# Optimization experiments

Measured on AMD Instinct MI355X. Metric: run time of the kernel, lower is better.

The kernel has to match this reference:

```python
import jax, jax.numpy as jnp
import numpy as np

N_ROLES = 6
EPS = 1e-5

def _ln(x, scale, bias):
    m = jnp.mean(x, axis=-1, keepdims=True)
    v = jnp.var(x, axis=-1, keepdims=True)
    return (x - m) * jax.lax.rsqrt(v + EPS) * scale + bias

def setup_inputs() -> dict:
    key = jax.random.key(0)
    ks = jax.random.split(key, 20)
    T, B, D_OBS, H, A = 32, 1024, 256, 512, 32
    inp = {
        'rnn_states': jax.random.normal(ks[0], (B, H), jnp.float32),
        'obs': jax.random.normal(ks[1], (T, B, D_OBS), jnp.float32),
        'resets': jnp.zeros((T, B), jnp.float32),
        'available_actions': jnp.ones((T, B, A), jnp.float32),
        'role_ids': jax.random.randint(ks[2], (T, B), 0, N_ROLES, jnp.int32),
        # feature norm over obs_dim
        'fn_scale': jnp.ones((D_OBS,), jnp.float32),
        'fn_bias': jnp.zeros((D_OBS,), jnp.float32),
        # base MLP: obs_dim->512->512, each followed by LayerNorm
        'W0': jax.random.normal(ks[3], (D_OBS, H), jnp.float32) * 0.02,
        'b0': jnp.zeros((H,), jnp.float32),
        'ln0_scale': jnp.ones((H,), jnp.float32),
        'ln0_bias': jnp.zeros((H,), jnp.float32),
        'W1': jax.random.normal(ks[4], (H, H), jnp.float32) * 0.02,
        'b1': jnp.zeros((H,), jnp.float32),
        'ln1_scale': jnp.ones((H,), jnp.float32),
        'ln1_bias': jnp.zeros((H,), jnp.float32),
        # per-role routes: obs_dim->128->H (stacked over roles)
        'Wr0': jax.random.normal(ks[5], (N_ROLES, D_OBS, 128), jnp.float32) * 0.02,
        'br0': jnp.zeros((N_ROLES, 128), jnp.float32),
        'Wr1': jax.random.normal(ks[6], (N_ROLES, 128, H), jnp.float32) * 0.02,
        'br1': jnp.zeros((N_ROLES, H), jnp.float32),
        # per-role heads: H->64->32->action_dim (stacked over roles)
        'Wh0': jax.random.normal(ks[7], (N_ROLES, H, 64), jnp.float32) * 0.02,
        'bh0': jnp.zeros((N_ROLES, 64), jnp.float32),
        'Wh1': jax.random.normal(ks[8], (N_ROLES, 64, 32), jnp.float32) * 0.02,
        'bh1': jnp.zeros((N_ROLES, 32), jnp.float32),
        'Wh2': jax.random.normal(ks[9], (N_ROLES, 32, A), jnp.float32) * 0.02,
        'bh2': jnp.zeros((N_ROLES, A), jnp.float32),
    }
    return inp

def _gather_by_role(all_values, role_ids):
    # all_values: (K, T, B, F); role_ids: (T, B) -> (T, B, F)
    idx = role_ids[None, :, :, None].astype(jnp.int32)
    return jnp.take_along_axis(all_values, idx, axis=0)[0]

def reference(rnn_states, obs, resets, available_actions, role_ids,
              fn_scale, fn_bias, W0, b0, ln0_scale, ln0_bias,
              W1, b1, ln1_scale, ln1_bias,
              Wr0, br0, Wr1, br1,
              Wh0, bh0, Wh1, bh1, Wh2, bh2):
    # feature normalization on raw obs
    obs_n = _ln(obs, fn_scale, fn_bias)
    # shared base MLP (relu + LayerNorm after each Dense)
    e = _ln(jax.nn.relu(obs_n @ W0 + b0), ln0_scale, ln0_bias)
    e = _ln(jax.nn.relu(e @ W1 + b1), ln1_scale, ln1_bias)
    # per-role pre-GRU residual routes on (normalized) obs
    r = jax.nn.relu(jnp.einsum('tbi,kih->ktbh', obs_n, Wr0) + br0[:, None, None, :])
    r = jax.nn.relu(jnp.einsum('ktbh,kho->ktbo', r, Wr1) + br1[:, None, None, :])
    e = e + _gather_by_role(r, role_ids)
    # no recurrent policy configured: rnn_states pass through
    # per-role heads -> all logits (K, T, B, A)
    h = jax.nn.relu(jnp.einsum('tbh,khf->ktbf', e, Wh0) + bh0[:, None, None, :])
    h = jax.nn.relu(jnp.einsum('ktbf,kfg->ktbg', h, Wh1) + bh1[:, None, None, :])
    all_logits = jnp.einsum('ktbg,kga->ktba', h, Wh2) + bh2[:, None, None, :]
    logits = _gather_by_role(all_logits, role_ids)
    logits = jnp.where(available_actions > 0.5, logits, jnp.full_like(logits, -1e10))
    return rnn_states, logits
```

## Files before the change

### kernel.cpp

```cpp
#include <hip/hip_runtime.h>
#include <stdint.h>

typedef unsigned short u16;
typedef unsigned int u32;

using bf16x8 = __attribute__((ext_vector_type(8))) short;
using f32x4  = __attribute__((ext_vector_type(4))) float;

#define DEVINL __device__ __forceinline__

DEVINL float b2f(u16 u) { return __builtin_bit_cast(float, (u32)u << 16); }
DEVINL u16 f2b(float f) {
  u32 u = __builtin_bit_cast(u32, f);
  u += 0x7FFFu + ((u >> 16) & 1u);
  return (u16)(u >> 16);
}

DEVINL void gll16(const u16* src, u16* dst) {
  __builtin_amdgcn_global_load_lds(
      (const __attribute__((address_space(1))) void*)(uintptr_t)src,
      (__attribute__((address_space(3))) void*)(uintptr_t)dst, 16, 0, 0);
}

DEVINL void tp_tile(const float* __restrict__ s, u16* __restrict__ d,
                    int R, int C, int bx, int by, int z)
{
  __shared__ u16 tile[32][33];
  const size_t mstride = (size_t)R * C;
  s += (size_t)z * mstride;
  d += (size_t)z * mstride;
  int r0 = bx * 32, c0 = by * 32;
  int tx = threadIdx.x & 31, ty = threadIdx.x >> 5;
#pragma unroll
  for (int i = 0; i < 32; i += 8)
    tile[ty + i][tx] = f2b(s[(size_t)(r0 + ty + i) * C + (c0 + tx)]);
  __syncthreads();
#pragma unroll
  for (int i = 0; i < 32; i += 8)
    d[(size_t)(c0 + ty + i) * R + (r0 + tx)] = tile[tx][ty + i];
}

__global__ __launch_bounds__(256) void transpose_all(
    const float* W0, const float* W1, const float* Wr0, const float* Wr1, const float* Wh0,
    u16* W0t, u16* W1t, u16* Wr0t, u16* Wr1t, u16* Wh0t)
{
  int b = blockIdx.x;
  if (b < 128)      {            tp_tile(W0, W0t, 256, 512, b % 8,  b / 8, 0); }
  else if (b < 384) { b -= 128;  tp_tile(W1, W1t, 512, 512, b % 16, b / 16, 0); }
  else if (b < 576) { b -= 384;  int t = b / 8;  tp_tile(Wr0, Wr0t, 256, 128, b % 8,  t % 4,  t / 4); }
  else if (b < 960) { b -= 576;  int t = b / 4;  tp_tile(Wr1, Wr1t, 128, 512, b % 4,  t % 16, t / 16); }
  else              { b -= 960;  int t = b / 16; tp_tile(Wh0, Wh0t, 512, 64,  b % 16, t % 2,  t / 2); }
}

__global__ __launch_bounds__(256) void ln_f32_256(
    const float* __restrict__ X, const float* __restrict__ sc,
    const float* __restrict__ bi, u16* __restrict__ Y, int nrows)
{
  constexpr int D = 256, PER = 4;
  int lane = threadIdx.x & 63;
  int row = blockIdx.x * 4 + (threadIdx.x >> 6);
  if (row >= nrows) return;
  const float* xr = X + (size_t)row * D + lane * PER;
  float x[PER] __attribute__((aligned(16)));
  *(float4*)x = *(const float4*)xr;
  float s = 0.f, s2 = 0.f;
#pragma unroll
  for (int p = 0; p < PER; ++p) { s += x[p]; s2 += x[p] * x[p]; }
#pragma unroll
  for (int o = 32; o > 0; o >>= 1) { s += __shfl_xor(s, o, 64); s2 += __shfl_xor(s2, o, 64); }
  float m = s * (1.f / D);
  float v = s2 * (1.f / D) - m * m;
  float inv = rsqrtf(v + 1e-5f);
  u16 yu[PER] __attribute__((aligned(8)));
#pragma unroll
  for (int p = 0; p < PER; ++p)
    yu[p] = f2b((x[p] - m) * inv * sc[lane * PER + p] + bi[lane * PER + p]);
  *(uint2*)(Y + (size_t)row * D + lane * PER) = *(uint2*)yu;
}

#define NROLE 6
__global__ __launch_bounds__(256) void role_count(
    const int* __restrict__ rid, int* __restrict__ blkCnt)
{
  __shared__ int h[NROLE];
  if (threadIdx.x < NROLE) h[threadIdx.x] = 0;
  __syncthreads();
  int i = blockIdx.x * 256 + threadIdx.x;
  atomicAdd(&h[rid[i]], 1);
  __syncthreads();
  if (threadIdx.x < NROLE) blkCnt[blockIdx.x * NROLE + threadIdx.x] = h[threadIdx.x];
}

__global__ __launch_bounds__(256) void role_scan(
    const int* __restrict__ blkCnt, int* __restrict__ blkBase,
    int* __restrict__ baseArr, int* __restrict__ cntArr)
{
  __shared__ int c[128 * NROLE];
  __shared__ int bb[128 * NROLE];
  __shared__ int sbase[NROLE], scnt[NROLE];
  for (int i = threadIdx.x; i < 128 * NROLE; i += 256) c[i] = blkCnt[i];
  __syncthreads();
  if (threadIdx.x < NROLE) {
    int k = threadIdx.x, run = 0;
    for (int b = 0; b < 128; ++b) { bb[b * NROLE + k] = run; run += c[b * NROLE + k]; }
    scnt[k] = run;
  }
  __syncthreads();
  if (threadIdx.x == 0) {
    int r = 0;
    for (int k = 0; k < NROLE; ++k) { sbase[k] = r; r += scnt[k]; }
  }
  __syncthreads();
  if (threadIdx.x < NROLE) { baseArr[threadIdx.x] = sbase[threadIdx.x]; cntArr[threadIdx.x] = scnt[threadIdx.x]; }
  for (int i = threadIdx.x; i < 128 * NROLE; i += 256)
    blkBase[i] = bb[i] + sbase[i % NROLE];
}

__global__ __launch_bounds__(256) void role_fill(
    const int* __restrict__ rid, const int* __restrict__ blkBase, int* __restrict__ bucket)
{
  __shared__ int h[NROLE];
  if (threadIdx.x < NROLE) h[threadIdx.x] = 0;
  __syncthreads();
  int i = blockIdx.x * 256 + threadIdx.x;
  int k = rid[i];
  int pos = atomicAdd(&h[k], 1);
  bucket[blkBase[blockIdx.x * NROLE + k] + pos] = i;
}

template <int K>
__global__ __launch_bounds__(256, 2) void gemm_ln(
    const u16* __restrict__ A, const u16* __restrict__ Bt,
    const float* __restrict__ bias, const float* __restrict__ lnsc,
    const float* __restrict__ lnbi, u16* __restrict__ C)
{
  constexpr int BK = 64, NI = K / BK;
  __shared__ __align__(16) u16 As[2][64 * BK];
  __shared__ float redS[64][4];
  __shared__ float redSS[64][4];
  __shared__ float prm[1536];
  const int tid = threadIdx.x;
  const int rowBase = blockIdx.x * 64;
  const int lane = tid & 63, wave = tid >> 6;
#pragma unroll
  for (int i = tid; i < 512; i += 256) {
    prm[i] = bias[i]; prm[512 + i] = lnsc[i]; prm[1024 + i] = lnbi[i];
  }
  u32 aOff[2];
#pragma unroll
  for (int r = 0; r < 2; ++r) {
    int row = r * 32 + (tid >> 3);
    aOff[r] = (u32)(rowBase + row) * (u32)K + (u32)(((tid & 7) ^ (row & 7)) * 8);
  }
  const int quad = lane >> 4, lm = lane & 15, l7 = lm & 7;
  const int wn = wave * 128;
  u32 bOff[8];
#pragma unroll
  for (int j = 0; j < 8; ++j)
    bOff[j] = (u32)(wn + j * 16 + lm) * (u32)K + (u32)(quad * 8);

  f32x4 acc[4][8] = {};

#pragma unroll
  for (int r = 0; r < 2; ++r)
    gll16(A + aOff[r], &As[0][r * 2048 + wave * 512]);
  bf16x8 bP[8];
#pragma unroll
  for (int j = 0; j < 8; ++j)
    bP[j] = *(const bf16x8*)(Bt + bOff[j]);
  __syncthreads();

  for (int i = 0; i < NI; ++i) {
    const u16* Ab = As[i & 1];
    if (i + 1 < NI) {
#pragma unroll
      for (int r = 0; r < 2; ++r)
        gll16(A + aOff[r] + (i + 1) * BK, &As[(i + 1) & 1][r * 2048 + wave * 512]);
    }
    bf16x8 bN[8];
#pragma unroll
    for (int j = 0; j < 8; ++j)
      bN[j] = *(const bf16x8*)(Bt + bOff[j] + i * BK + 32);
    bf16x8 af[4];
#pragma unroll
    for (int i2 = 0; i2 < 4; ++i2)
      af[i2] = *(const bf16x8*)&Ab[(i2 * 16 + lm) * 64 + ((quad ^ l7) * 8)];
#pragma unroll
    for (int i2 = 0; i2 < 4; ++i2)
#pragma unroll
      for (int j = 0; j < 8; ++j)
        acc[i2][j] = __builtin_amdgcn_mfma_f32_16x16x32_bf16(af[i2], bP[j], acc[i2][j], 0, 0, 0);
    if (i + 1 < NI) {
#pragma unroll
      for (int j = 0; j < 8; ++j)
        bP[j] = *(const bf16x8*)(Bt + bOff[j] + (i + 1) * BK);
    }
#pragma unroll
    for (int i2 = 0; i2 < 4; ++i2)
      af[i2] = *(const bf16x8*)&Ab[(i2 * 16 + lm) * 64 + (((quad + 4) ^ l7) * 8)];
#pragma unroll
    for (int i2 = 0; i2 < 4; ++i2)
#pragma unroll
      for (int j = 0; j < 8; ++j)
        acc[i2][j] = __builtin_amdgcn_mfma_f32_16x16x32_bf16(af[i2], bN[j], acc[i2][j], 0, 0, 0);
    __syncthreads();
  }

#pragma unroll
  for (int i2 = 0; i2 < 4; ++i2) {
#pragma unroll
    for (int r2 = 0; r2 < 4; ++r2) {
      float s = 0.f, ss = 0.f;
#pragma unroll
      for (int j = 0; j < 8; ++j) {
        float v = fmaxf(acc[i2][j][r2] + prm[wn + j * 16 + lm], 0.f);
        acc[i2][j][r2] = v;
        s += v; ss += v * v;
      }
#pragma unroll
      for (int o = 1; o < 16; o <<= 1) { s += __shfl_xor(s, o, 64); ss += __shfl_xor(ss, o, 64); }
      if (lm == 0) {
        int rowL = i2 * 16 + quad * 4 + r2;
        redS[rowL][wave] = s;
        redSS[rowL][wave] = ss;
      }
    }
  }
  __syncthreads();
#pragma unroll
  for (int i2 = 0; i2 < 4; ++i2) {
#pragma unroll
    for (int r2 = 0; r2 < 4; ++r2) {
      int rowL = i2 * 16 + quad * 4 + r2;
      float ts  = redS[rowL][0] + redS[rowL][1] + redS[rowL][2] + redS[rowL][3];
      float tss = redSS[rowL][0] + redSS[rowL][1] + redSS[rowL][2] + redSS[rowL][3];
      float m = ts * (1.f / 512.f);
      float var = tss * (1.f / 512.f) - m * m;
      float inv = rsqrtf(var + 1e-5f);
      size_t base = (size_t)(rowBase + rowL) * 512;
#pragma unroll
      for (int j = 0; j < 8; ++j) {
        int col = wn + j * 16 + lm;
        float y = (acc[i2][j][r2] - m) * inv * prm[512 + col] + prm[1024 + col];
        C[base + col] = f2b(y);
      }
    }
  }
}

__global__ __launch_bounds__(256, 3) void route_head(
    const u16* __restrict__ obs_n, const u16* __restrict__ e,
    const u16* __restrict__ Wr0t, const float* __restrict__ br0,
    const u16* __restrict__ Wr1t, const float* __restrict__ br1,
    const u16* __restrict__ Wh0t, const float* __restrict__ bh0,
    const float* __restrict__ Wh1, const float* __restrict__ bh1,
    const float* __restrict__ Wh2, const float* __restrict__ bh2,
    const float* __restrict__ avail,
    const int* __restrict__ bucket, const int* __restrict__ baseArr,
    const int* __restrict__ cntArr, float* __restrict__ outLogits)
{
  __shared__ __align__(16) u16 sm[20480];
  __shared__ float prm[704];
  __shared__ float h1s[32 * 36];
  const int tid = threadIdx.x;

  int role = 0, rem = blockIdx.x, cnt;
  for (;;) {
    cnt = cntArr[role];
    int tiles = (cnt + 31) >> 5;
    if (rem < tiles) break;
    rem -= tiles;
    if (++role >= NROLE) return;
  }
  const int limit = cnt;
  const int rowBase = rem * 32;
  const int roleBase = baseArr[role];

  {
    const float* s0 = br0 + role * 128;
    const float* s1 = br1 + role * 512;
    const float* s2 = bh0 + role * 64;
    if (tid < 128) prm[tid] = s0[tid];
    for (int i = tid; i < 512; i += 256) prm[128 + i] = s1[i];
    if (tid < 64) prm[640 + tid] = s2[tid];
  }

  const int lane = tid & 63, wave = tid >> 6;
  const int quad = lane >> 4, lm = lane & 15, l7 = lm & 7;

#pragma unroll
  for (int r = 0; r < 4; ++r) {
    int lrow = r * 8 + (tid >> 5);
    int i = rowBase + lrow;
    if (i >= limit) i = rowBase;
    int grow = bucket[roleBase + i];
    gll16(obs_n + (u32)grow * 256u + (u32)((((tid & 31) ^ (lrow & 7)) * 8)),
          &sm[r * 2048 + wave * 512]);
  }
  __syncthreads();

  const int wn0 = wave * 32;
  const u16* B0 = Wr0t + (size_t)role * 128 * 256;
  f32x4 acc0[2][2] = {};
#pragma unroll
  for (int kk = 0; kk < 256; kk += 32) {
    const int kc = kk >> 3;
    bf16x8 af[2], bf0[2];
#pragma unroll
    for (int i2 = 0; i2 < 2; ++i2)
      af[i2] = *(const bf16x8*)&sm[(i2 * 16 + lm) * 256 + (((quad + kc) ^ l7) * 8)];
#pragma unroll
    for (int j = 0; j < 2; ++j)
      bf0[j] = *(const bf16x8*)(B0 + (u32)(wn0 + j * 16 + lm) * 256u + (u32)(quad * 8 + kk));
#pragma unroll
    for (int i2 = 0; i2 < 2; ++i2)
#pragma unroll
      for (int j = 0; j < 2; ++j)
        acc0[i2][j] = __builtin_amdgcn_mfma_f32_16x16x32_bf16(af[i2], bf0[j], acc0[i2][j], 0, 0, 0);
  }
  u16* r1 = sm + 16384;
#pragma unroll
  for (int i2 = 0; i2 < 2; ++i2) {
#pragma unroll
    for (int r2 = 0; r2 < 4; ++r2) {
      int row = i2 * 16 + quad * 4 + r2;
#pragma unroll
      for (int j = 0; j < 2; ++j) {
        int col = wn0 + j * 16 + lm;
        float v = fmaxf(acc0[i2][j][r2] + prm[col], 0.f);
        r1[row * 128 + (((col >> 3) ^ (row & 7)) * 8) + (col & 7)] = f2b(v);
      }
    }
  }
  __syncthreads();

  const int wn1 = wave * 128;
  const u16* B1 = Wr1t + (size_t)role * 512 * 128;
  f32x4 acc1[2][8] = {};
#pragma unroll
  for (int kk = 0; kk < 128; kk += 32) {
    const int kc = kk >> 3;
    bf16x8 af[2], bf1[8];
#pragma unroll
    for (int i2 = 0; i2 < 2; ++i2)
      af[i2] = *(const bf16x8*)&r1[(i2 * 16 + lm) * 128 + (((quad + kc) ^ l7) * 8)];
#pragma unroll
    for (int j = 0; j < 8; ++j)
      bf1[j] = *(const bf16x8*)(B1 + (u32)(wn1 + j * 16 + lm) * 128u + (u32)(quad * 8 + kk));
#pragma unroll
    for (int i2 = 0; i2 < 2; ++i2)
#pragma unroll
      for (int j = 0; j < 8; ++j)
        acc1[i2][j] = __builtin_amdgcn_mfma_f32_16x16x32_bf16(af[i2], bf1[j], acc1[i2][j], 0, 0, 0);
  }
#pragma unroll
  for (int i2 = 0; i2 < 2; ++i2) {
#pragma unroll
    for (int r2 = 0; r2 < 4; ++r2) {
      int row = i2 * 16 + quad * 4 + r2;
      int i = rowBase + row;
      int ic = (i < limit) ? i : (limit - 1);
      u32 grow = (u32)bucket[roleBase + ic];
#pragma unroll
      for (int j = 0; j < 8; ++j) {
        int col = wn1 + j * 16 + lm;
        float v = fmaxf(acc1[i2][j][r2] + prm[128 + col], 0.f) + b2f(e[(size_t)grow * 512 + col]);
        sm[row * 512 + (((col >> 3) ^ (row & 7)) * 8) + (col & 7)] = f2b(v);
      }
    }
  }
  __syncthreads();

  const int wn2 = wave * 16;
  const u16* B2 = Wh0t + (size_t)role * 64 * 512;
  f32x4 acc2[2] = {};
#pragma unroll
  for (int kk = 0; kk < 512; kk += 32) {
    const int kc = kk >> 3;
    bf16x8 af[2], bf2;
#pragma unroll
    for (int i2 = 0; i2 < 2; ++i2)
      af[i2] = *(const bf16x8*)&sm[(i2 * 16 + lm) * 512 + (((quad + kc) ^ l7) * 8)];
    bf2 = *(const bf16x8*)(B2 + (u32)(wn2 + lm) * 512u + (u32)(quad * 8 + kk));
#pragma unroll
    for (int i2 = 0; i2 < 2; ++i2)
      acc2[i2] = __builtin_amdgcn_mfma_f32_16x16x32_bf16(af[i2], bf2, acc2[i2], 0, 0, 0);
  }
  u16* h0s = sm + 16384;
#pragma unroll
  for (int i2 = 0; i2 < 2; ++i2) {
#pragma unroll
    for (int r2 = 0; r2 < 4; ++r2) {
      int row = i2 * 16 + quad * 4 + r2;
      int col = wn2 + lm;
      h0s[row * 68 + col] = f2b(fmaxf(acc2[i2][r2] + prm[640 + col], 0.f));
    }
  }
  __syncthreads();

  {
    const int r = tid >> 3;
    const int n0 = (tid & 7) * 4;
    const bool valid = (rowBase + r) < limit;
    const float* W1k = Wh1 + (size_t)role * 64 * 32;
    const float* W2k = Wh2 + (size_t)role * 32 * 32;
    float4 a1 = *(const float4*)(bh1 + role * 32 + n0);
#pragma unroll 8
    for (int j = 0; j < 64; ++j) {
      float hj = b2f(h0s[r * 68 + j]);
      float4 wv = *(const float4*)(W1k + j * 32 + n0);
      a1.x += hj * wv.x; a1.y += hj * wv.y; a1.z += hj * wv.z; a1.w += hj * wv.w;
    }
    h1s[r * 36 + n0 + 0] = fmaxf(a1.x, 0.f);
    h1s[r * 36 + n0 + 1] = fmaxf(a1.y, 0.f);
    h1s[r * 36 + n0 + 2] = fmaxf(a1.z, 0.f);
    h1s[r * 36 + n0 + 3] = fmaxf(a1.w, 0.f);
    __syncthreads();
    float4 a2 = *(const float4*)(bh2 + role * 32 + n0);
#pragma unroll 8
    for (int n = 0; n < 32; ++n) {
      float hn = h1s[r * 36 + n];
      float4 wv = *(const float4*)(W2k + n * 32 + n0);
      a2.x += hn * wv.x; a2.y += hn * wv.y; a2.z += hn * wv.z; a2.w += hn * wv.w;
    }
    if (valid) {
      int g = bucket[roleBase + rowBase + r];
      float4 av = *(const float4*)(avail + (size_t)g * 32 + n0);
      float4 o;
      o.x = (av.x > 0.5f) ? a2.x : -1e10f;
      o.y = (av.y > 0.5f) ? a2.y : -1e10f;
      o.z = (av.z > 0.5f) ? a2.z : -1e10f;
      o.w = (av.w > 0.5f) ? a2.w : -1e10f;
      *(float4*)(outLogits + (size_t)g * 32 + n0) = o;
    }
  }
}

extern "C" void kernel_launch(void* const* d_in, const int* in_sizes, int n_in,
                              void* d_out, int out_size, void* d_ws, size_t ws_size,
                              hipStream_t stream)
{
  const float* rnn  = (const float*)d_in[0];
  const float* obs  = (const float*)d_in[1];
  const float* avail= (const float*)d_in[3];
  const int*   rid  = (const int*)d_in[4];
  const float* fn_s = (const float*)d_in[5];
  const float* fn_b = (const float*)d_in[6];
  const float* W0   = (const float*)d_in[7];
  const float* b0   = (const float*)d_in[8];
  const float* ln0s = (const float*)d_in[9];
  const float* ln0b = (const float*)d_in[10];
  const float* W1   = (const float*)d_in[11];
  const float* b1   = (const float*)d_in[12];
  const float* ln1s = (const float*)d_in[13];
  const float* ln1b = (const float*)d_in[14];
  const float* Wr0  = (const float*)d_in[15];
  const float* br0  = (const float*)d_in[16];
  const float* Wr1  = (const float*)d_in[17];
  const float* br1  = (const float*)d_in[18];
  const float* Wh0  = (const float*)d_in[19];
  const float* bh0  = (const float*)d_in[20];
  const float* Wh1  = (const float*)d_in[21];
  const float* bh1  = (const float*)d_in[22];
  const float* Wh2  = (const float*)d_in[23];
  const float* bh2  = (const float*)d_in[24];

  const int ROWS = 32768;

  char* w = (char*)d_ws;
  auto carve = [&](size_t bytes) { char* p = w; w += (bytes + 255) & ~(size_t)255; return p; };
  u16* obs_n  = (u16*)carve((size_t)ROWS * 256 * 2);
  u16* bufA   = (u16*)carve((size_t)ROWS * 512 * 2);
  u16* bufB   = (u16*)carve((size_t)ROWS * 512 * 2);
  u16* W0t    = (u16*)carve((size_t)512 * 256 * 2);
  u16* W1t    = (u16*)carve((size_t)512 * 512 * 2);
  u16* Wr0t   = (u16*)carve((size_t)6 * 128 * 256 * 2);
  u16* Wr1t   = (u16*)carve((size_t)6 * 512 * 128 * 2);
  u16* Wh0t   = (u16*)carve((size_t)6 * 64 * 512 * 2);
  int* bucket = (int*)carve((size_t)ROWS * 4);
  int* blkCnt = (int*)carve((size_t)128 * NROLE * 4);
  int* blkBase= (int*)carve((size_t)128 * NROLE * 4);
  int* baseArr= (int*)carve(256);
  int* cntArr = (int*)carve(256);

  float* outLogits = (float*)d_out + (size_t)1024 * 512;

  hipMemcpyAsync(d_out, rnn, (size_t)1024 * 512 * 4, hipMemcpyDeviceToDevice, stream);

  transpose_all<<<1152, 256, 0, stream>>>(W0, W1, Wr0, Wr1, Wh0, W0t, W1t, Wr0t, Wr1t, Wh0t);

  ln_f32_256<<<8192, 256, 0, stream>>>(obs, fn_s, fn_b, obs_n, ROWS);

  role_count<<<128, 256, 0, stream>>>(rid, blkCnt);
  role_scan<<<1, 256, 0, stream>>>(blkCnt, blkBase, baseArr, cntArr);
  role_fill<<<128, 256, 0, stream>>>(rid, blkBase, bucket);

  gemm_ln<256><<<512, 256, 0, stream>>>(obs_n, W0t, b0, ln0s, ln0b, bufA);
  gemm_ln<512><<<512, 256, 0, stream>>>(bufA, W1t, b1, ln1s, ln1b, bufB);

  route_head<<<1029, 256, 0, stream>>>(obs_n, bufB, Wr0t, br0, Wr1t, br1, Wh0t, bh0,
                                       Wh1, bh1, Wh2, bh2, avail,
                                       bucket, baseArr, cntArr, outLogits);
}
```

Before: 274.6 us.

## Prefetch e rows into LDS and double-buffer weight fragments in route_head

The route_head kernel now loads the gathered e rows for its 32-row tile into shared memory with async global-to-LDS copies, issued alongside the obs_n tile. The residual add then reads them from LDS instead of doing scattered per-element global loads after the second GEMM. Each of the three MFMA loops also prefetches the next k-step's weight fragments into registers before the current MFMAs run. Shared memory grows from about 40KB to 56KB and the launch-bounds occupancy hint drops from 3 to 2 blocks, so fewer blocks may be resident per CU.

```diff
diff --git a/kernel.cpp b/kernel.cpp
--- a/kernel.cpp
+++ b/kernel.cpp
@@ -21,6 +21,8 @@
       (const __attribute__((address_space(1))) void*)(uintptr_t)src,
       (__attribute__((address_space(3))) void*)(uintptr_t)dst, 16, 0, 0);
 }
+
+#define MFMA __builtin_amdgcn_mfma_f32_16x16x32_bf16
 
 DEVINL void tp_tile(const float* __restrict__ s, u16* __restrict__ d,
                     int R, int C, int bx, int by, int z)
@@ -189,7 +191,7 @@
     for (int i2 = 0; i2 < 4; ++i2)
 #pragma unroll
       for (int j = 0; j < 8; ++j)
-        acc[i2][j] = __builtin_amdgcn_mfma_f32_16x16x32_bf16(af[i2], bP[j], acc[i2][j], 0, 0, 0);
+        acc[i2][j] = MFMA(af[i2], bP[j], acc[i2][j], 0, 0, 0);
     if (i + 1 < NI) {
 #pragma unroll
       for (int j = 0; j < 8; ++j)
@@ -202,7 +204,7 @@
     for (int i2 = 0; i2 < 4; ++i2)
 #pragma unroll
       for (int j = 0; j < 8; ++j)
-        acc[i2][j] = __builtin_amdgcn_mfma_f32_16x16x32_bf16(af[i2], bN[j], acc[i2][j], 0, 0, 0);
+        acc[i2][j] = MFMA(af[i2], bN[j], acc[i2][j], 0, 0, 0);
     __syncthreads();
   }
 
@@ -248,7 +250,7 @@
   }
 }
 
-__global__ __launch_bounds__(256, 3) void route_head(
+__global__ __launch_bounds__(256, 2) void route_head(
     const u16* __restrict__ obs_n, const u16* __restrict__ e,
     const u16* __restrict__ Wr0t, const float* __restrict__ br0,
     const u16* __restrict__ Wr1t, const float* __restrict__ br1,
@@ -259,7 +261,7 @@
     const int* __restrict__ bucket, const int* __restrict__ baseArr,
     const int* __restrict__ cntArr, float* __restrict__ outLogits)
 {
-  __shared__ __align__(16) u16 sm[20480];
+  __shared__ __align__(16) u16 sm[28672];
   __shared__ float prm[704];
   __shared__ float h1s[32 * 36];
   const int tid = threadIdx.x;
@@ -276,15 +278,6 @@
   const int rowBase = rem * 32;
   const int roleBase = baseArr[role];
 
-  {
-    const float* s0 = br0 + role * 128;
-    const float* s1 = br1 + role * 512;
-    const float* s2 = bh0 + role * 64;
-    if (tid < 128) prm[tid] = s0[tid];
-    for (int i = tid; i < 512; i += 256) prm[128 + i] = s1[i];
-    if (tid < 64) prm[640 + tid] = s2[tid];
-  }
-
   const int lane = tid & 63, wave = tid >> 6;
   const int quad = lane >> 4, lm = lane & 15, l7 = lm & 7;
 
@@ -294,31 +287,55 @@
     int i = rowBase + lrow;
     if (i >= limit) i = rowBase;
     int grow = bucket[roleBase + i];
-    gll16(obs_n + (u32)grow * 256u + (u32)((((tid & 31) ^ (lrow & 7)) * 8)),
+    gll16(obs_n + (u32)grow * 256u + (u32)(((tid & 31) ^ (lrow & 7)) * 8),
+          &sm[16384 + r * 2048 + wave * 512]);
+  }
+#pragma unroll
+  for (int r = 0; r < 8; ++r) {
+    int lrow = r * 4 + wave;
+    int i = rowBase + lrow;
+    if (i >= limit) i = rowBase;
+    int grow = bucket[roleBase + i];
+    int chunk = tid & 63;
+    int sw = (chunk & 56) | ((chunk ^ lrow) & 7);
+    gll16(e + (u32)grow * 512u + (u32)(sw * 8),
           &sm[r * 2048 + wave * 512]);
+  }
+  {
+    if (tid < 128) prm[tid] = br0[role * 128 + tid];
+    for (int i = tid; i < 512; i += 256) prm[128 + i] = br1[role * 512 + i];
+    if (tid < 64) prm[640 + tid] = bh0[role * 64 + tid];
   }
   __syncthreads();
 
   const int wn0 = wave * 32;
   const u16* B0 = Wr0t + (size_t)role * 128 * 256;
   f32x4 acc0[2][2] = {};
+  bf16x8 b0P[2];
+#pragma unroll
+  for (int j = 0; j < 2; ++j)
+    b0P[j] = *(const bf16x8*)(B0 + (u32)(wn0 + j * 16 + lm) * 256u + (u32)(quad * 8));
 #pragma unroll
   for (int kk = 0; kk < 256; kk += 32) {
+    bf16x8 b0N[2];
+    if (kk + 32 < 256) {
+#pragma unroll
+      for (int j = 0; j < 2; ++j)
+        b0N[j] = *(const bf16x8*)(B0 + (u32)(wn0 + j * 16 + lm) * 256u + (u32)(quad * 8 + kk + 32));
+    }
     const int kc = kk >> 3;
-    bf16x8 af[2], bf0[2];
+    bf16x8 af[2];
 #pragma unroll
     for (int i2 = 0; i2 < 2; ++i2)
-      af[i2] = *(const bf16x8*)&sm[(i2 * 16 + lm) * 256 + (((quad + kc) ^ l7) * 8)];
-#pragma unroll
-    for (int j = 0; j < 2; ++j)
-      bf0[j] = *(const bf16x8*)(B0 + (u32)(wn0 + j * 16 + lm) * 256u + (u32)(quad * 8 + kk));
+      af[i2] = *(const bf16x8*)&sm[16384 + (i2 * 16 + lm) * 256 + (((quad + kc) ^ l7) * 8)];
 #pragma unroll
     for (int i2 = 0; i2 < 2; ++i2)
 #pragma unroll
       for (int j = 0; j < 2; ++j)
-        acc0[i2][j] = __builtin_amdgcn_mfma_f32_16x16x32_bf16(af[i2], bf0[j], acc0[i2][j], 0, 0, 0);
-  }
-  u16* r1 = sm + 16384;
+        acc0[i2][j] = MFMA(af[i2], b0P[j], acc0[i2][j], 0, 0, 0);
+    if (kk + 32 < 256) { b0P[0] = b0N[0]; b0P[1] = b0N[1]; }
+  }
+  u16* r1 = sm + 24576;
 #pragma unroll
   for (int i2 = 0; i2 < 2; ++i2) {
 #pragma unroll
@@ -337,35 +354,44 @@
   const int wn1 = wave * 128;
   const u16* B1 = Wr1t + (size_t)role * 512 * 128;
   f32x4 acc1[2][8] = {};
+  bf16x8 b1P[8];
+#pragma unroll
+  for (int j = 0; j < 8; ++j)
+    b1P[j] = *(const bf16x8*)(B1 + (u32)(wn1 + j * 16 + lm) * 128u + (u32)(quad * 8));
 #pragma unroll
   for (int kk = 0; kk < 128; kk += 32) {
+    bf16x8 b1N[8];
+    if (kk + 32 < 128) {
+#pragma unroll
+      for (int j = 0; j < 8; ++j)
+        b1N[j] = *(const bf16x8*)(B1 + (u32)(wn1 + j * 16 + lm) * 128u + (u32)(quad * 8 + kk + 32));
+    }
     const int kc = kk >> 3;
-    bf16x8 af[2], bf1[8];
+    bf16x8 af[2];
 #pragma unroll
     for (int i2 = 0; i2 < 2; ++i2)
       af[i2] = *(const bf16x8*)&r1[(i2 * 16 + lm) * 128 + (((quad + kc) ^ l7) * 8)];
 #pragma unroll
-    for (int j = 0; j < 8; ++j)
-      bf1[j] = *(const bf16x8*)(B1 + (u32)(wn1 + j * 16 + lm) * 128u + (u32)(quad * 8 + kk));
-#pragma unroll
     for (int i2 = 0; i2 < 2; ++i2)
 #pragma unroll
       for (int j = 0; j < 8; ++j)
-        acc1[i2][j] = __builtin_amdgcn_mfma_f32_16x16x32_bf16(af[i2], bf1[j], acc1[i2][j], 0, 0, 0);
+        acc1[i2][j] = MFMA(af[i2], b1P[j], acc1[i2][j], 0, 0, 0);
+    if (kk + 32 < 128) {
+#pragma unroll
+      for (int j = 0; j < 8; ++j) b1P[j] = b1N[j];
+    }
   }
 #pragma unroll
   for (int i2 = 0; i2 < 2; ++i2) {
 #pragma unroll
     for (int r2 = 0; r2 < 4; ++r2) {
       int row = i2 * 16 + quad * 4 + r2;
-      int i = rowBase + row;
-      int ic = (i < limit) ? i : (limit - 1);
-      u32 grow = (u32)bucket[roleBase + ic];
 #pragma unroll
       for (int j = 0; j < 8; ++j) {
         int col = wn1 + j * 16 + lm;
-        float v = fmaxf(acc1[i2][j][r2] + prm[128 + col], 0.f) + b2f(e[(size_t)grow * 512 + col]);
-        sm[row * 512 + (((col >> 3) ^ (row & 7)) * 8) + (col & 7)] = f2b(v);
+        int addr = row * 512 + (((col >> 3) ^ (row & 7)) * 8) + (col & 7);
+        float v = fmaxf(acc1[i2][j][r2] + prm[128 + col], 0.f) + b2f(sm[addr]);
+        sm[addr] = f2b(v);
       }
     }
   }
@@ -374,17 +400,21 @@
   const int wn2 = wave * 16;
   const u16* B2 = Wh0t + (size_t)role * 64 * 512;
   f32x4 acc2[2] = {};
+  bf16x8 b2P = *(const bf16x8*)(B2 + (u32)(wn2 + lm) * 512u + (u32)(quad * 8));
 #pragma unroll
   for (int kk = 0; kk < 512; kk += 32) {
+    bf16x8 b2N;
+    if (kk + 32 < 512)
+      b2N = *(const bf16x8*)(B2 + (u32)(wn2 + lm) * 512u + (u32)(quad * 8 + kk + 32));
     const int kc = kk >> 3;
-    bf16x8 af[2], bf2;
+    bf16x8 af[2];
 #pragma unroll
     for (int i2 = 0; i2 < 2; ++i2)
       af[i2] = *(const bf16x8*)&sm[(i2 * 16 + lm) * 512 + (((quad + kc) ^ l7) * 8)];
-    bf2 = *(const bf16x8*)(B2 + (u32)(wn2 + lm) * 512u + (u32)(quad * 8 + kk));
 #pragma unroll
     for (int i2 = 0; i2 < 2; ++i2)
-      acc2[i2] = __builtin_amdgcn_mfma_f32_16x16x32_bf16(af[i2], bf2, acc2[i2], 0, 0, 0);
+      acc2[i2] = MFMA(af[i2], b2P, acc2[i2], 0, 0, 0);
+    if (kk + 32 < 512) b2P = b2N;
   }
   u16* h0s = sm + 16384;
 #pragma unroll
```

Measured after the change: 280.6 us. +2.2%, slower.
